# Kernel optimization log

Measured on AMD Instinct MI355X. Metric: run time of the kernel, lower is better.

## Reference

```python
import jax, jax.numpy as jnp
import numpy as np
from jax import lax

H_IMG, W_IMG = 1280, 1280
STRIDES = (8, 16, 32, 64, 128)
FEAT_SHAPES = tuple((H_IMG // s) * (W_IMG // s) for s in STRIDES)  # (25600,6400,1600,400,100)
N_POINTS = sum(FEAT_SHAPES)  # 34100
NUM_CLASSES = 1
TOPK = 1000
SCORE_THRESH = 0.05
NMS_THRESH = 0.5
MAX_DET = 300
BATCH = 8
N_GT = 200


def make_points():
    # matches AnchorFreePS.reference_points: cell centers at stride*i + stride//2, (cx, cy) order
    pts = []
    for s in STRIDES:
        h, w = H_IMG // s, W_IMG // s
        cx = np.arange(w, dtype=np.float32) * s + s // 2
        cy = np.arange(h, dtype=np.float32) * s + s // 2
        gy, gx = np.meshgrid(cy, cx, indexing='ij')
        pts.append(np.stack([gx, gy], axis=-1).reshape(-1, 2))
    return jnp.asarray(np.concatenate(pts, axis=0))


def setup_inputs() -> dict:
    key = jax.random.key(0)
    k1, k2, k3, k4 = jax.random.split(key, 4)
    points = make_points()  # [N,2]
    xy = jax.random.uniform(k1, (BATCH, N_GT, 2), minval=0.0, maxval=1000.0)
    wh = jax.random.uniform(k2, (BATCH, N_GT, 2), minval=20.0, maxval=260.0)
    gt_boxes = jnp.concatenate([xy, xy + wh], axis=-1)  # [B,M,4] x1y1x2y2
    cls_logits = jax.random.normal(k3, (BATCH, N_POINTS, NUM_CLASSES)) * 1.5 - 3.0
    regression = jax.random.uniform(k4, (BATCH, N_POINTS, 4)) * 0.1  # normalized ltrb codes
    return {"points": points, "gt_boxes": gt_boxes, "cls_logits": cls_logits, "regression": regression}


def match_points_to_boxes(points, gt_boxes):
    # point-in-box test + area-cost argmin (compute_loss matched_idxs)
    px = points[None, :, None, 0]  # [1,N,1]
    py = points[None, :, None, 1]
    b = gt_boxes[:, None, :, :]    # [B,1,M,4]
    inside = (px >= b[..., 0]) & (px <= b[..., 2]) & (py >= b[..., 1]) & (py <= b[..., 3])  # [B,N,M]
    matched = jnp.any(inside, axis=-1)  # [B,N]
    areas = (gt_boxes[..., 2] - gt_boxes[..., 0]) * (gt_boxes[..., 3] - gt_boxes[..., 1])  # [B,M]
    BIG = jnp.float32(2 ** 31 - 1)  # torch.iinfo(torch.int).max
    cost = jnp.where(inside, areas[:, None, :], BIG)
    idx = jnp.argmin(cost, axis=-1)
    return jnp.where(matched, idx, -1)


def decode_boxes(rel, pts):
    # FCOSBoxCoder.decode_single with weights (1,1,1,1)
    l = rel[:, 0] * W_IMG
    t = rel[:, 1] * H_IMG
    r = rel[:, 2] * W_IMG
    b = rel[:, 3] * H_IMG
    x, y = pts[:, 0], pts[:, 1]
    return jnp.stack([x - l, y - t, x + r, y + b], axis=-1)


def clip_boxes(boxes):
    return jnp.stack([
        jnp.clip(boxes[:, 0], 0.0, W_IMG),
        jnp.clip(boxes[:, 1], 0.0, H_IMG),
        jnp.clip(boxes[:, 2], 0.0, W_IMG),
        jnp.clip(boxes[:, 3], 0.0, H_IMG)], axis=-1)


def nms(boxes, scores, labels, valid_init):
    # fixed-size sequential NMS equivalent to batched_nms (same-label suppression)
    work = lax.stop_gradient(jnp.where(valid_init, scores, -jnp.inf))

    def body(w, _):
        i = jnp.argmax(w)
        s = w[i]
        box = boxes[i]
        x1 = jnp.maximum(box[0], boxes[:, 0])
        y1 = jnp.maximum(box[1], boxes[:, 1])
        x2 = jnp.minimum(box[2], boxes[:, 2])
        y2 = jnp.minimum(box[3], boxes[:, 3])
        inter = jnp.clip(x2 - x1, 0.0) * jnp.clip(y2 - y1, 0.0)
        a1 = (box[2] - box[0]) * (box[3] - box[1])
        a2 = (boxes[:, 2] - boxes[:, 0]) * (boxes[:, 3] - boxes[:, 1])
        iou = inter / (a1 + a2 - inter + 1e-9)
        supp = (iou > NMS_THRESH) & (labels == labels[i])
        w = jnp.where(supp, -jnp.inf, w).at[i].set(-jnp.inf)
        return w, (i, s)

    _, (idxs, picked) = lax.scan(body, work, None, length=MAX_DET)
    valid = picked > -jnp.inf
    return idxs, valid


def postprocess_image(points, cls_i, reg_i):
    bx_list, sc_list, lb_list = [], [], []
    off = 0
    for size in FEAT_SHAPES:  # fixed small level loop
        sl = slice(off, off + size)
        off += size
        scores = jax.nn.sigmoid(cls_i[sl]).reshape(-1)  # [size*C]
        k = min(TOPK, size * NUM_CLASSES)
        sc, idx = lax.top_k(scores, k)
        a = idx // NUM_CLASSES
        lb = idx % NUM_CLASSES
        bx = clip_boxes(decode_boxes(reg_i[sl][a], points[sl][a]))
        bx_list.append(bx)
        sc_list.append(sc)
        lb_list.append(lb)
    boxes = jnp.concatenate(bx_list, axis=0)
    scores = jnp.concatenate(sc_list, axis=0)
    labels = jnp.concatenate(lb_list, axis=0)
    idxs, valid = nms(boxes, scores, labels, scores > SCORE_THRESH)
    out_boxes = jnp.where(valid[:, None], boxes[idxs], 0.0)
    out_scores = jnp.where(valid, scores[idxs], 0.0)
    out_labels = jnp.where(valid, labels[idxs], -1)
    return out_boxes, out_scores, out_labels, valid


def reference(points, gt_boxes, cls_logits, regression):
    matched_idxs = match_points_to_boxes(points, gt_boxes)  # [B,N]
    boxes, scores, labels, valid = jax.vmap(
        lambda c, r: postprocess_image(points, c, r))(cls_logits, regression)
    return matched_idxs, boxes, scores, labels, valid
```

## Files before the change

kernel.cpp:

```cpp
#include <hip/hip_runtime.h>
#include <stdint.h>

#define N_POINTS   34100
#define BATCH      8
#define N_GT       200
#define NLEV       5
#define NCAND      3500
#define MAX_DET    300
#define SCORE_TH   0.05f
#define NMS_TH     0.5f
#define IMG        1280.0f
#define NBIN       4096
#define TIE_CAP    4096
#define MTH 0.50000002980232238769531250

#define OUT_MATCH  0
#define OUT_BOXES  272800
#define OUT_SCORES 282400
#define OUT_LABELS 284800
#define OUT_VALID  287200

#define WS_KEYS    0
#define WS_SBOX    2632192
#define WS_SSC     3080192
#define WS_MASK    3192192
#define WS_DIAG    9500032
#define WS_HIST    WS_MASK
#define HSUB       8
#define MASK_STRIDE 98560
#define DIAG_STRIDE 3520


typedef unsigned long long u64;
typedef uint32_t u32;

__device__ __forceinline__ int mask_off(int c) {
    int g = c >> 6;
    return 64 * (55 * g - (g * (g - 1)) / 2) + (c - (g << 6)) * (55 - g);
}

__device__ __forceinline__ int level_of(int p) {
    return (p < 25600) ? 0 : (p < 32000) ? 1 : (p < 33600) ? 2 : (p < 34000) ? 3 : 4;
}
__device__ __forceinline__ int loff_of(int l) {
    return (l == 0) ? 0 : (l == 1) ? 25600 : (l == 2) ? 32000 : (l == 3) ? 33600 : 34000;
}
__device__ __forceinline__ int k_of(int l) {
    return (l == 0) ? 1000 : (l == 1) ? 1000 : (l == 2) ? 1000 : (l == 3) ? 400 : 100;
}
__device__ __forceinline__ u64 readlane64(u64 v, int t) {
    u32 lo = (u32)__builtin_amdgcn_readlane((int)(u32)v, t);
    u32 hi = (u32)__builtin_amdgcn_readlane((int)(u32)(v >> 32), t);
    return ((u64)hi << 32) | lo;
}

#define MPT 2
__global__ __launch_bounds__(256)
void match_key_kernel(const float* __restrict__ points,
                      const float* __restrict__ gt,
                      float* __restrict__ out_match) {
#pragma clang fp contract(off)
    __shared__ float bx1[N_GT], by1[N_GT], bx2[N_GT], by2[N_GT], ar[N_GT];
    const int b = blockIdx.y;
    const int base = blockIdx.x * (256 * MPT) + threadIdx.x;

    for (int j = threadIdx.x; j < N_GT; j += 256) {
        float x1 = gt[(b * N_GT + j) * 4 + 0];
        float y1 = gt[(b * N_GT + j) * 4 + 1];
        float x2 = gt[(b * N_GT + j) * 4 + 2];
        float y2 = gt[(b * N_GT + j) * 4 + 3];
        bx1[j] = x1; by1[j] = y1; bx2[j] = x2; by2[j] = y2;
        ar[j] = (x2 - x1) * (y2 - y1);
    }
    __syncthreads();

    const float BIGF = 2147483648.0f;
    float px[MPT], py[MPT], best[MPT];
    int bi[MPT];
#pragma unroll
    for (int k = 0; k < MPT; ++k) {
        int p = base + k * 256;
        int pc = (p < N_POINTS) ? p : 0;
        px[k] = points[pc * 2 + 0];
        py[k] = points[pc * 2 + 1];
        best[k] = BIGF; bi[k] = -1;
    }
    for (int j = 0; j < N_GT; ++j) {
        float x1 = bx1[j], y1 = by1[j], x2 = bx2[j], y2 = by2[j], a = ar[j];
#pragma unroll
        for (int k = 0; k < MPT; ++k) {
            bool inside = (px[k] >= x1) && (px[k] <= x2) &&
                          (py[k] >= y1) && (py[k] <= y2);
            float cost = inside ? a : BIGF;
            if (cost < best[k]) { best[k] = cost; bi[k] = j; }
        }
    }
#pragma unroll
    for (int k = 0; k < MPT; ++k) {
        int p = base + k * 256;
        if (p >= N_POINTS) continue;
        out_match[b * N_POINTS + p] = (float)bi[k];
    }
}

__global__ __launch_bounds__(1024)
void hist_kernel(const float* __restrict__ logits,
                 u32* __restrict__ keys,
                 u32* __restrict__ ghist) {
#pragma clang fp contract(off)
    __shared__ u32 hh[NBIN];
    const int b = blockIdx.x & 7;
    const int f = blockIdx.x >> 3;
    const int tid = threadIdx.x;
    int lev, sub, p0, cnt;
    if (f < 8)       { lev = 0; sub = f;     p0 = f * 3200;             cnt = 3200; }
    else if (f < 10) { lev = 1; sub = f - 8; p0 = 25600 + (f - 8) * 3200; cnt = 3200; }
    else if (f == 10){ lev = 2; sub = 0;     p0 = 32000;                cnt = 1600; }
    else if (f == 11){ lev = 3; sub = 0;     p0 = 33600;                cnt = 400;  }
    else             { lev = 4; sub = 0;     p0 = 34000;                cnt = 100;  }

    for (int i = tid; i < NBIN; i += 1024) hh[i] = 0u;
    __syncthreads();

    for (int i = tid; i < cnt; i += 1024) {
        int p = p0 + i;
        float lg = logits[b * N_POINTS + p];
        float s = 1.0f / (1.0f + expf(-lg));
        u32 u = __float_as_uint(s);
        u32 key = (u & 0x80000000u) ? ~u : (u | 0x80000000u);
        keys[b * N_POINTS + p] = key;
        atomicAdd(&hh[(key >> 19) & 4095u], 1u);
    }
    __syncthreads();

    u32* outp = ghist + (((u32)b * NLEV + (u32)lev) * HSUB + (u32)sub) * NBIN;
    for (int i = tid; i < NBIN; i += 1024) outp[i] = hh[i];
}

#define SORT_T 1024
#define LSWZ(j) (((j) & 63) * 65 + ((j) >> 6))
__global__ __launch_bounds__(SORT_T)
void pipeline_kernel(const u32* __restrict__ keys,
                     const u32* __restrict__ ghist,
                     const float* __restrict__ reg,
                     const float* __restrict__ points,
                     float* __restrict__ sboxes,
                     float* __restrict__ sscores) {
#pragma clang fp contract(off)
    __shared__ __align__(16) char smem[131072];
    u64* sk   = (u64*)smem;
    u64* tb   = (u64*)(smem + 32768);
    u64* aux  = (u64*)(smem + 65536);
    u32* h    = (u32*)(smem + 98304);
    u32* bs   = (u32*)(smem + 114688);
    u32* lsb  = (u32*)smem;
    __shared__ u32 sTl[NLEV], skkl[NLEV], wt[16];
    __shared__ u32 scnt, stcnt;

    const int b = blockIdx.x;
    const int tid = threadIdx.x;
    const int lane = tid & 63;
    const int wid = tid >> 6;
    const u32* kk_ = keys + b * N_POINTS;

    if (tid == 0) { scnt = 0u; stcnt = 0u; }

    {
        const u32* hb = ghist + (u32)b * (NLEV * HSUB * NBIN);
#pragma unroll
        for (int lev = 0; lev < NLEV; ++lev) {
            const int SUBS = (lev == 0) ? 8 : (lev == 1) ? 2 : 1;
            const u32* hl = hb + lev * HSUB * NBIN + tid;
            u32 s0 = 0, s1 = 0, s2 = 0, s3 = 0;
#pragma unroll
            for (int sub = 0; sub < SUBS; ++sub) {
                const u32* hs = hl + sub * NBIN;
                s0 += hs[0]; s1 += hs[1024]; s2 += hs[2048]; s3 += hs[3072];
            }
            u32* lv = lsb + lev * 4160;
            lv[LSWZ(tid)]        = s0;
            lv[LSWZ(tid + 1024)] = s1;
            lv[LSWZ(tid + 2048)] = s2;
            lv[LSWZ(tid + 3072)] = s3;
        }
        const uint4* kp4 = (const uint4*)kk_;
        u32 wacc = 0;
        for (int i = tid; i < 8525; i += SORT_T) {
            uint4 v = kp4[i];
            wacc ^= v.x ^ v.y ^ v.z ^ v.w;
        }
        asm volatile("" :: "v"(wacc));
    }
    __syncthreads();

    if (wid < NLEV) {
        const u32 K = (u32)k_of(wid);
        const u32* hh = lsb + wid * 4160;
        u32 S = 0;
#pragma unroll 16
        for (int i = 0; i < 64; ++i) S += hh[i * 65 + lane];
        u32 acc = S;
#pragma unroll
        for (int off = 1; off < 64; off <<= 1) {
            u32 v = (u32)__shfl_down((int)acc, off);
            if (lane + off < 64) acc += v;
        }
        u32 sfxAfter = acc - S;
        bool hit = (sfxAfter < K) && (sfxAfter + S >= K);
        u64 bal = __ballot(hit);
        int Lg = (int)__builtin_ctzll(bal);
        u32 sfxG = (u32)__shfl((int)sfxAfter, Lg);

        u32 v = hh[lane * 65 + Lg];
        u32 acc2 = v;
#pragma unroll
        for (int off = 1; off < 64; off <<= 1) {
            u32 t = (u32)__shfl_down((int)acc2, off);
            if (lane + off < 64) acc2 += t;
        }
        u32 sfx2 = sfxG + acc2 - v;
        bool hit2 = (sfx2 < K) && (sfx2 + v >= K);
        if (hit2) { sTl[wid] = (u32)(Lg * 64 + lane); skkl[wid] = K - sfx2; }
    }
    __syncthreads();

    const u64 below = (lane == 0) ? 0ull : (~0ull >> (64 - lane));
    const int CHUNK = 4 * SORT_T;
    for (int it = 0; it < (N_POINTS + CHUNK - 1) / CHUNK; ++it) {
        u32 key4[4]; int pc4[4]; bool act4[4];
#pragma unroll
        for (int u = 0; u < 4; ++u) {
            int i = it * CHUNK + u * SORT_T + tid;
            act4[u] = (i < N_POINTS);
            pc4[u] = act4[u] ? i : (N_POINTS - 1);
            key4[u] = kk_[pc4[u]];
        }
#pragma unroll
        for (int u = 0; u < 4; ++u) {
            bool active = act4[u];
            int pc = pc4[u];
            u32 key = key4[u];
            int l = level_of(pc);
            u32 digit = (key >> 19) & 4095u;
            u32 T = sTl[l];
            bool isDef = active && (digit > T);
            bool isTie = active && (digit == T);
            u64 k50 = ((u64)key << 18) | ((u64)(7 - l) << 15)
                    | (u64)(32767 - (pc - loff_of(l)));
            u64 grp = __ballot(isDef);
            if (grp) {
                int leader = (int)__builtin_ctzll(grp);
                u32 base_ = 0;
                if (lane == leader)
                    base_ = atomicAdd(&scnt, (u32)__builtin_popcountll(grp));
                base_ = (u32)__shfl((int)base_, leader);
                if (isDef) sk[base_ + (u32)__builtin_popcountll(grp & below)] = k50;
            }
            u64 tg = __ballot(isTie);
            if (tg) {
                int leader = (int)__builtin_ctzll(tg);
                u32 base_ = 0;
                if (lane == leader)
                    base_ = atomicAdd(&stcnt, (u32)__builtin_popcountll(tg));
                base_ = (u32)__shfl((int)base_, leader);
                if (isTie) {
                    u32 pos = base_ + (u32)__builtin_popcountll(tg & below);
                    if (pos < TIE_CAP) tb[pos] = k50;
                }
            }
        }
    }
    __syncthreads();

    int t = (int)stcnt; if (t > TIE_CAP) t = TIE_CAP;
    for (int j0 = tid; j0 - tid < t; j0 += SORT_T) {
        bool active = j0 < t;
        u64 kj = active ? tb[j0] : 0ull;
        u32 lvtag = (u32)(kj >> 15) & 7u;
        int r = 0;
        for (int i = 0; i < t; ++i) {
            u64 ki = tb[i];
            r += (ki > kj && (((u32)(ki >> 15) & 7u) == lvtag)) ? 1 : 0;
        }
        bool inc = active && (r < (int)skkl[7 - lvtag]);
        u64 grp = __ballot(inc);
        if (grp) {
            int leader = (int)__builtin_ctzll(grp);
            u32 base_ = 0;
            if (lane == leader)
                base_ = atomicAdd(&scnt, (u32)__builtin_popcountll(grp));
            base_ = (u32)__shfl((int)base_, leader);
            if (inc) sk[base_ + (u32)__builtin_popcountll(grp & below)] = kj;
        }
    }
    __syncthreads();
    const int total = (int)scnt;

    for (int i = tid; i < NBIN; i += SORT_T) h[i] = 0u;
    __syncthreads();
    for (int i = tid; i < total; i += SORT_T)
        atomicAdd(&h[(u32)(sk[i] >> 37) & 4095u], 1u);
    __syncthreads();

    u32 t0 = h[4095 - 4 * tid];
    u32 t1 = h[4095 - (4 * tid + 1)];
    u32 t2 = h[4095 - (4 * tid + 2)];
    u32 t3 = h[4095 - (4 * tid + 3)];
    u32 tsum = t0 + t1 + t2 + t3;
    u32 sc_ = tsum;
#pragma unroll
    for (int off = 1; off < 64; off <<= 1) {
        u32 v = (u32)__shfl_up((int)sc_, off);
        if (lane >= off) sc_ += v;
    }
    if (lane == 63) wt[wid] = sc_;
    __syncthreads();
    if (tid < 64) {
        u32 v = (tid < 16) ? wt[tid] : 0u;
        u32 s2 = v;
#pragma unroll
        for (int off = 1; off < 16; off <<= 1) {
            u32 x = (u32)__shfl_up((int)s2, off);
            if (tid >= off) s2 += x;
        }
        if (tid < 16) wt[tid] = s2 - v;
    }
    __syncthreads();
    u32 run = (sc_ - tsum) + wt[wid];
    bs[4095 - 4 * tid] = run;       run += t0;
    bs[4095 - (4 * tid + 1)] = run; run += t1;
    bs[4095 - (4 * tid + 2)] = run; run += t2;
    bs[4095 - (4 * tid + 3)] = run;
    __syncthreads();
    for (int i = tid; i < NBIN; i += SORT_T) h[i] = 0u;
    __syncthreads();
    for (int i = tid; i < total; i += SORT_T) {
        u64 k = sk[i];
        u32 d = (u32)(k >> 37) & 4095u;
        u32 pos = bs[d] + atomicAdd(&h[d], 1u);
        aux[pos] = k;
    }
    __syncthreads();
    for (int p = tid; p < total; p += SORT_T) {
        u64 kp = aux[p];
        u32 d = (u32)(kp >> 37) & 4095u;
        u32 gbase = bs[d];
        u32 gend = (d == 0) ? (u32)total : bs[d - 1];
        u32 r = 0;
        for (u32 q = gbase; q < gend; ++q) r += (aux[q] > kp) ? 1u : 0u;
        sk[gbase + r] = kp;
    }
    __syncthreads();

    for (int r = tid; r < NCAND; r += SORT_T) {
        float x1 = 0.f, y1 = 0.f, x2 = 0.f, y2 = 0.f, sc = 0.f;
        if (r < total) {
            u64 k50 = sk[r];
            int lowb = (int)(k50 & 0x3FFFFull);
            int l = 7 - (lowb >> 15);
            int idxl = 32767 - (lowb & 32767);
            int p = loff_of(l) + idxl;
            u32 key32 = (u32)(k50 >> 18);
            sc = __uint_as_float(key32 ^ 0x80000000u);
            int gp = b * N_POINTS + p;
            float l_ = reg[gp * 4 + 0] * IMG;
            float t_ = reg[gp * 4 + 1] * IMG;
            float r_ = reg[gp * 4 + 2] * IMG;
            float bb = reg[gp * 4 + 3] * IMG;
            float px = points[p * 2 + 0];
            float py = points[p * 2 + 1];
            x1 = fminf(fmaxf(px - l_, 0.0f), IMG);
            y1 = fminf(fmaxf(py - t_, 0.0f), IMG);
            x2 = fminf(fmaxf(px + r_, 0.0f), IMG);
            y2 = fminf(fmaxf(py + bb, 0.0f), IMG);
        }
        int slot = b * NCAND + r;
        sboxes[slot * 4 + 0] = x1;
        sboxes[slot * 4 + 1] = y1;
        sboxes[slot * 4 + 2] = x2;
        sboxes[slot * 4 + 3] = y2;
        sscores[slot] = sc;
    }
}

__global__ __launch_bounds__(256)
void mask_kernel(const float* __restrict__ sboxes,
                 const float* __restrict__ sscores,
                 u64* __restrict__ mask,
                 u64* __restrict__ diag) {
#pragma clang fp contract(off)
    const int b = blockIdx.x & 7;
    const int gx = blockIdx.x >> 3;
    const int wv = threadIdx.x >> 6;
    const int lane = threadIdx.x & 63;
    const int NG = (NCAND + 3) >> 2;
    const int NH = (NG + 1) >> 1;
    const int gidx = gx * 4 + wv;
    if (gidx >= NH) return;

    const float4* gb = (const float4*)sboxes + b * NCAND;
    const float* gs = sscores + b * NCAND;
    u64* mout = mask + (size_t)b * MASK_STRIDE;
    u64* dout = diag + (size_t)b * DIAG_STRIDE;

    for (int s = 0; s < 2; ++s) {
        const int g0 = (s == 0) ? gidx : (NG - 1 - gidx);
        if (s == 1 && g0 == gidx) break;
        const int c0 = g0 << 2;

        float4 bc[4]; float a1[4]; bool ok[4]; int g[4]; u64* rp[4];
        bool any = false;
#pragma unroll
        for (int i = 0; i < 4; ++i) {
            int c = c0 + i;
            int cc = (c < NCAND) ? c : (NCAND - 1);
            bc[i] = gb[cc];
            a1[i] = (bc[i].z - bc[i].x) * (bc[i].w - bc[i].y);
            ok[i] = (c < NCAND) && (gs[cc] > SCORE_TH);
            g[i] = cc >> 6;
            rp[i] = mout + mask_off(cc) - g[i];
            any |= ok[i];
        }
        if (!any) continue;

        for (int w = (c0 >> 6); w < 55; ++w) {
            int cj = (w << 6) + lane;
            float4 bj = (cj < NCAND) ? gb[cj] : make_float4(0.f, 0.f, 0.f, 0.f);
            float a2 = (bj.z - bj.x) * (bj.w - bj.y);
#pragma unroll
            for (int i = 0; i < 4; ++i) {
                float x1 = fmaxf(bc[i].x, bj.x);
                float y1 = fmaxf(bc[i].y, bj.y);
                float x2 = fminf(bc[i].z, bj.z);
                float y2 = fminf(bc[i].w, bj.w);
                float inter = fmaxf(x2 - x1, 0.f) * fmaxf(y2 - y1, 0.f);
                float denom = a1[i] + a2 - inter + 1e-9f;
                float hf = 0.5f * denom;
                float rr = fmaf(0x1p-25f, denom, hf);
                u64 bits = __ballot(inter > rr);
                u64 eq = __ballot(inter == rr);
                if (eq) {
                    u64 fb = __ballot((double)inter > MTH * (double)denom);
                    bits |= (eq & fb);
                }
                if (lane == 0 && ok[i] && w >= g[i]) {
                    rp[i][w] = bits;
                    if (w == g[i]) dout[c0 + i] = bits;
                }
            }
        }
    }
}

__global__ __launch_bounds__(1024)
void scan_kernel(const float* __restrict__ sboxes,
                 const float* __restrict__ sscores,
                 const u64* __restrict__ mask,
                 const u64* __restrict__ diag,
                 float* __restrict__ out) {
    __shared__ u32 pick_idx[MAX_DET];
    const int b = blockIdx.x;
    const int tid = threadIdx.x;
    const u64* mrow = mask + (size_t)b * MASK_STRIDE;
    const u64* drow = diag + (size_t)b * DIAG_STRIDE;

    if (tid >= 64) {
        const uint4* mp = (const uint4*)mrow;
        const uint4* dp = (const uint4*)drow;
        const int t = tid - 64;
        u32 a0 = 0, a1 = 0, a2 = 0, a3 = 0;
        int i = t;
        for (; i + 2880 < 49280; i += 3840) {
            uint4 v0 = mp[i];
            uint4 v1 = mp[i + 960];
            uint4 v2 = mp[i + 1920];
            uint4 v3 = mp[i + 2880];
            a0 ^= v0.x ^ v0.y ^ v0.z ^ v0.w;
            a1 ^= v1.x ^ v1.y ^ v1.z ^ v1.w;
            a2 ^= v2.x ^ v2.y ^ v2.z ^ v2.w;
            a3 ^= v3.x ^ v3.y ^ v3.z ^ v3.w;
        }
        for (; i < 49280; i += 960) {
            uint4 v = mp[i];
            a0 ^= v.x ^ v.y ^ v.z ^ v.w;
        }
        if (t < 880) {
            uint4 v0 = dp[t];
            uint4 v1 = dp[t + 880];
            a1 ^= v0.x ^ v0.y ^ v0.z ^ v0.w;
            a2 ^= v1.x ^ v1.y ^ v1.z ^ v1.w;
        }
        u32 acc = a0 ^ a1 ^ a2 ^ a3;
        asm volatile("" :: "v"(acc));
        return;
    }

    const int lane = tid;
    const float4* gb = (const float4*)sboxes + b * NCAND;
    const float* gs = sscores + b * NCAND;

    float* ob = out + OUT_BOXES  + b * MAX_DET * 4;
    float* os = out + OUT_SCORES + b * MAX_DET;
    float* ol = out + OUT_LABELS + b * MAX_DET;
    float* ov = out + OUT_VALID  + b * MAX_DET;

    u64 m = 0ull;
    u64 rowN = drow[lane];
    float sjN = gs[lane];

    int kept = 0;
    for (int w = 0; w < 55; ++w) {
        const int wbase = w << 6;
        const u64 row = rowN;
        const float sj = sjN;
        if (w < 54) {
            int cn = wbase + 64 + lane;
            int cc = (cn < NCAND) ? cn : (NCAND - 1);
            rowN = drow[cc];
            float s = gs[cc];
            sjN = (cn < NCAND) ? s : 0.f;
        }
        int c = wbase + lane;
        u64 bad = __ballot(!((c < NCAND) && (sj > SCORE_TH)));
        u64 cur = readlane64(m, w) | bad;
        u64 km = 0ull;
        while (kept < MAX_DET) {
            u64 avail = ~cur;
            if (avail == 0ull) break;
            int t = (int)__builtin_ctzll(avail);
            u64 r = readlane64(row, t);
            cur |= r | (1ull << t);
            km |= 1ull << t;
            if (lane == 0) pick_idx[kept] = (u32)(wbase + t);
            kept++;
        }
        if (km) {
            const bool lr = (lane >= w && lane < 55);
            const int lo = lane - w;
            u64 acc = 0ull;
            while (km) {
#define POPBIT(tn) int tn = -1; if (km) { tn = (int)__builtin_ctzll(km); km &= km - 1ull; }
                POPBIT(t0) POPBIT(t1) POPBIT(t2) POPBIT(t3)
                POPBIT(t4) POPBIT(t5) POPBIT(t6) POPBIT(t7)
#undef POPBIT
                u64 v0 = 0, v1 = 0, v2 = 0, v3 = 0, v4 = 0, v5 = 0, v6 = 0, v7 = 0;
                if (lr) {
                    v0 = mrow[mask_off(wbase + t0) + lo];
                    if (t1 >= 0) v1 = mrow[mask_off(wbase + t1) + lo];
                    if (t2 >= 0) v2 = mrow[mask_off(wbase + t2) + lo];
                    if (t3 >= 0) v3 = mrow[mask_off(wbase + t3) + lo];
                    if (t4 >= 0) v4 = mrow[mask_off(wbase + t4) + lo];
                    if (t5 >= 0) v5 = mrow[mask_off(wbase + t5) + lo];
                    if (t6 >= 0) v6 = mrow[mask_off(wbase + t6) + lo];
                    if (t7 >= 0) v7 = mrow[mask_off(wbase + t7) + lo];
                }
                acc |= ((v0 | v1) | (v2 | v3)) | ((v4 | v5) | (v6 | v7));
            }
            m |= acc;
        }
        if (kept >= MAX_DET) break;
    }

    for (int k = lane; k < kept; k += 64) {
        u32 c = pick_idx[k];
        float4 bx = gb[c];
        float s = gs[c];
        ob[k * 4 + 0] = bx.x;
        ob[k * 4 + 1] = bx.y;
        ob[k * 4 + 2] = bx.z;
        ob[k * 4 + 3] = bx.w;
        os[k] = s;
        ol[k] = 0.0f;
        ov[k] = 1.0f;
    }
    for (int k = kept + lane; k < MAX_DET; k += 64) {
        ob[k * 4 + 0] = 0.f; ob[k * 4 + 1] = 0.f;
        ob[k * 4 + 2] = 0.f; ob[k * 4 + 3] = 0.f;
        os[k] = 0.f; ol[k] = -1.f; ov[k] = 0.f;
    }
}

extern "C" void kernel_launch(void* const* d_in, const int* in_sizes, int n_in,
                              void* d_out, int out_size, void* d_ws, size_t ws_size,
                              hipStream_t stream) {
    const float* points = (const float*)d_in[0];
    const float* gt     = (const float*)d_in[1];
    const float* logits = (const float*)d_in[2];
    const float* reg    = (const float*)d_in[3];
    float* out = (float*)d_out;

    u32* keys      = (u32*)((char*)d_ws + WS_KEYS);
    float* sboxes  = (float*)((char*)d_ws + WS_SBOX);
    float* sscores = (float*)((char*)d_ws + WS_SSC);
    u64* mask   = (u64*)((char*)d_ws + WS_MASK);
    u64* diag   = (u64*)((char*)d_ws + WS_DIAG);
    u32* ghist  = (u32*)((char*)d_ws + WS_HIST);

    dim3 g1((N_POINTS + 256 * MPT - 1) / (256 * MPT), BATCH);
    match_key_kernel<<<g1, 256, 0, stream>>>(points, gt, out + OUT_MATCH);

    hist_kernel<<<13 * BATCH, 1024, 0, stream>>>(logits, keys, ghist);

    pipeline_kernel<<<BATCH, SORT_T, 0, stream>>>(keys, ghist, reg, points,
                                                  sboxes, sscores);

    mask_kernel<<<110 * BATCH, 256, 0, stream>>>(sboxes, sscores, mask, diag);

    scan_kernel<<<BATCH, 1024, 0, stream>>>(sboxes, sscores, mask, diag, out);
}
```

Before: 227.9 us.

## Merge match and histogram kernels, split threshold select from compaction kernel

Combines the point-to-box matching kernel and the score histogram kernel into one launch whose blocks branch by index, so the independent matching work and histogram work can run concurrently on the GPU. The histogram threshold selection moves out of the big pipeline kernel into its own small kernel that writes thresholds into spare workspace, and the compaction kernel reads them back. Cache-warming prefetch loops are widened to more loads in flight and extended to the box and score buffers. This adds an extra kernel launch and a global round-trip for the thresholds, and relies on an unused histogram slot as scratch space.

After: 230.0 us. No clear change (+0.9%).

```diff
diff --git a/kernel.cpp b/kernel.cpp
--- a/kernel.cpp
+++ b/kernel.cpp
@@ -54,116 +54,98 @@
     return ((u64)hi << 32) | lo;
 }
 
-#define MPT 2
-__global__ __launch_bounds__(256)
-void match_key_kernel(const float* __restrict__ points,
-                      const float* __restrict__ gt,
-                      float* __restrict__ out_match) {
+__global__ __launch_bounds__(1024)
+void match_hist_kernel(const float* __restrict__ points,
+                       const float* __restrict__ gt,
+                       const float* __restrict__ logits,
+                       float* __restrict__ out_match,
+                       u32* __restrict__ keys,
+                       u32* __restrict__ ghist) {
 #pragma clang fp contract(off)
     __shared__ float bx1[N_GT], by1[N_GT], bx2[N_GT], by2[N_GT], ar[N_GT];
-    const int b = blockIdx.y;
-    const int base = blockIdx.x * (256 * MPT) + threadIdx.x;
-
-    for (int j = threadIdx.x; j < N_GT; j += 256) {
-        float x1 = gt[(b * N_GT + j) * 4 + 0];
-        float y1 = gt[(b * N_GT + j) * 4 + 1];
-        float x2 = gt[(b * N_GT + j) * 4 + 2];
-        float y2 = gt[(b * N_GT + j) * 4 + 3];
-        bx1[j] = x1; by1[j] = y1; bx2[j] = x2; by2[j] = y2;
-        ar[j] = (x2 - x1) * (y2 - y1);
-    }
-    __syncthreads();
-
-    const float BIGF = 2147483648.0f;
-    float px[MPT], py[MPT], best[MPT];
-    int bi[MPT];
-#pragma unroll
-    for (int k = 0; k < MPT; ++k) {
-        int p = base + k * 256;
-        int pc = (p < N_POINTS) ? p : 0;
-        px[k] = points[pc * 2 + 0];
-        py[k] = points[pc * 2 + 1];
-        best[k] = BIGF; bi[k] = -1;
-    }
-    for (int j = 0; j < N_GT; ++j) {
-        float x1 = bx1[j], y1 = by1[j], x2 = bx2[j], y2 = by2[j], a = ar[j];
-#pragma unroll
-        for (int k = 0; k < MPT; ++k) {
-            bool inside = (px[k] >= x1) && (px[k] <= x2) &&
-                          (py[k] >= y1) && (py[k] <= y2);
-            float cost = inside ? a : BIGF;
-            if (cost < best[k]) { best[k] = cost; bi[k] = j; }
-        }
-    }
-#pragma unroll
-    for (int k = 0; k < MPT; ++k) {
-        int p = base + k * 256;
-        if (p >= N_POINTS) continue;
-        out_match[b * N_POINTS + p] = (float)bi[k];
-    }
-}
-
-__global__ __launch_bounds__(1024)
-void hist_kernel(const float* __restrict__ logits,
-                 u32* __restrict__ keys,
-                 u32* __restrict__ ghist) {
-#pragma clang fp contract(off)
     __shared__ u32 hh[NBIN];
     const int b = blockIdx.x & 7;
-    const int f = blockIdx.x >> 3;
+    const int g = blockIdx.x >> 3;
     const int tid = threadIdx.x;
-    int lev, sub, p0, cnt;
-    if (f < 8)       { lev = 0; sub = f;     p0 = f * 3200;             cnt = 3200; }
-    else if (f < 10) { lev = 1; sub = f - 8; p0 = 25600 + (f - 8) * 3200; cnt = 3200; }
-    else if (f == 10){ lev = 2; sub = 0;     p0 = 32000;                cnt = 1600; }
-    else if (f == 11){ lev = 3; sub = 0;     p0 = 33600;                cnt = 400;  }
-    else             { lev = 4; sub = 0;     p0 = 34000;                cnt = 100;  }
-
-    for (int i = tid; i < NBIN; i += 1024) hh[i] = 0u;
-    __syncthreads();
-
-    for (int i = tid; i < cnt; i += 1024) {
-        int p = p0 + i;
-        float lg = logits[b * N_POINTS + p];
-        float s = 1.0f / (1.0f + expf(-lg));
-        u32 u = __float_as_uint(s);
-        u32 key = (u & 0x80000000u) ? ~u : (u | 0x80000000u);
-        keys[b * N_POINTS + p] = key;
-        atomicAdd(&hh[(key >> 19) & 4095u], 1u);
-    }
-    __syncthreads();
-
-    u32* outp = ghist + (((u32)b * NLEV + (u32)lev) * HSUB + (u32)sub) * NBIN;
-    for (int i = tid; i < NBIN; i += 1024) outp[i] = hh[i];
-}
-
-#define SORT_T 1024
+
+    if (g < 17) {
+        const int base = g * 2048 + tid;
+        for (int j = tid; j < N_GT; j += 1024) {
+            float x1 = gt[(b * N_GT + j) * 4 + 0];
+            float y1 = gt[(b * N_GT + j) * 4 + 1];
+            float x2 = gt[(b * N_GT + j) * 4 + 2];
+            float y2 = gt[(b * N_GT + j) * 4 + 3];
+            bx1[j] = x1; by1[j] = y1; bx2[j] = x2; by2[j] = y2;
+            ar[j] = (x2 - x1) * (y2 - y1);
+        }
+        __syncthreads();
+
+        const float BIGF = 2147483648.0f;
+        float px[2], py[2], best[2];
+        int bi[2];
+#pragma unroll
+        for (int k = 0; k < 2; ++k) {
+            int p = base + k * 1024;
+            int pc = (p < N_POINTS) ? p : 0;
+            px[k] = points[pc * 2 + 0];
+            py[k] = points[pc * 2 + 1];
+            best[k] = BIGF; bi[k] = -1;
+        }
+        for (int j = 0; j < N_GT; ++j) {
+            float x1 = bx1[j], y1 = by1[j], x2 = bx2[j], y2 = by2[j], a = ar[j];
+#pragma unroll
+            for (int k = 0; k < 2; ++k) {
+                bool inside = (px[k] >= x1) && (px[k] <= x2) &&
+                              (py[k] >= y1) && (py[k] <= y2);
+                float cost = inside ? a : BIGF;
+                if (cost < best[k]) { best[k] = cost; bi[k] = j; }
+            }
+        }
+#pragma unroll
+        for (int k = 0; k < 2; ++k) {
+            int p = base + k * 1024;
+            if (p >= N_POINTS) continue;
+            out_match[b * N_POINTS + p] = (float)bi[k];
+        }
+    } else {
+        const int f = g - 17;
+        int lev, sub, p0, cnt;
+        if (f < 8)       { lev = 0; sub = f;     p0 = f * 3200;               cnt = 3200; }
+        else if (f < 10) { lev = 1; sub = f - 8; p0 = 25600 + (f - 8) * 3200; cnt = 3200; }
+        else if (f == 10){ lev = 2; sub = 0;     p0 = 32000;                  cnt = 1600; }
+        else if (f == 11){ lev = 3; sub = 0;     p0 = 33600;                  cnt = 400;  }
+        else             { lev = 4; sub = 0;     p0 = 34000;                  cnt = 100;  }
+
+        for (int i = tid; i < NBIN; i += 1024) hh[i] = 0u;
+        __syncthreads();
+
+        for (int i = tid; i < cnt; i += 1024) {
+            int p = p0 + i;
+            float lg = logits[b * N_POINTS + p];
+            float s = 1.0f / (1.0f + expf(-lg));
+            u32 u = __float_as_uint(s);
+            u32 key = (u & 0x80000000u) ? ~u : (u | 0x80000000u);
+            keys[b * N_POINTS + p] = key;
+            atomicAdd(&hh[(key >> 19) & 4095u], 1u);
+        }
+        __syncthreads();
+
+        u32* outp = ghist + (((u32)b * NLEV + (u32)lev) * HSUB + (u32)sub) * NBIN;
+        for (int i = tid; i < NBIN; i += 1024) outp[i] = hh[i];
+    }
+}
+
+#define SEL_OFF(b) ((((u32)(b) * NLEV + 4) * HSUB + 7) * NBIN)
+
 #define LSWZ(j) (((j) & 63) * 65 + ((j) >> 6))
-__global__ __launch_bounds__(SORT_T)
-void pipeline_kernel(const u32* __restrict__ keys,
-                     const u32* __restrict__ ghist,
-                     const float* __restrict__ reg,
-                     const float* __restrict__ points,
-                     float* __restrict__ sboxes,
-                     float* __restrict__ sscores) {
-#pragma clang fp contract(off)
-    __shared__ __align__(16) char smem[131072];
-    u64* sk   = (u64*)smem;
-    u64* tb   = (u64*)(smem + 32768);
-    u64* aux  = (u64*)(smem + 65536);
-    u32* h    = (u32*)(smem + 98304);
-    u32* bs   = (u32*)(smem + 114688);
-    u32* lsb  = (u32*)smem;
-    __shared__ u32 sTl[NLEV], skkl[NLEV], wt[16];
-    __shared__ u32 scnt, stcnt;
-
+__global__ __launch_bounds__(1024)
+void select_kernel(u32* __restrict__ ghist) {
+    __shared__ u32 lsb[5 * 4160];
+    __shared__ u32 sTl[NLEV], skkl[NLEV];
     const int b = blockIdx.x;
     const int tid = threadIdx.x;
     const int lane = tid & 63;
     const int wid = tid >> 6;
-    const u32* kk_ = keys + b * N_POINTS;
-
-    if (tid == 0) { scnt = 0u; stcnt = 0u; }
 
     {
         const u32* hb = ghist + (u32)b * (NLEV * HSUB * NBIN);
@@ -183,13 +165,6 @@
             lv[LSWZ(tid + 2048)] = s2;
             lv[LSWZ(tid + 3072)] = s3;
         }
-        const uint4* kp4 = (const uint4*)kk_;
-        u32 wacc = 0;
-        for (int i = tid; i < 8525; i += SORT_T) {
-            uint4 v = kp4[i];
-            wacc ^= v.x ^ v.y ^ v.z ^ v.w;
-        }
-        asm volatile("" :: "v"(wacc));
     }
     __syncthreads();
 
@@ -221,6 +196,66 @@
         u32 sfx2 = sfxG + acc2 - v;
         bool hit2 = (sfx2 < K) && (sfx2 + v >= K);
         if (hit2) { sTl[wid] = (u32)(Lg * 64 + lane); skkl[wid] = K - sfx2; }
+    }
+    __syncthreads();
+    if (tid < NLEV) {
+        u32* selp = ghist + SEL_OFF(b);
+        selp[tid] = sTl[tid];
+        selp[NLEV + tid] = skkl[tid];
+    }
+}
+
+#define SORT_T 1024
+__global__ __launch_bounds__(SORT_T)
+void compact_kernel(const u32* __restrict__ keys,
+                    const u32* __restrict__ ghist,
+                    const float* __restrict__ reg,
+                    const float* __restrict__ points,
+                    float* __restrict__ sboxes,
+                    float* __restrict__ sscores) {
+#pragma clang fp contract(off)
+    __shared__ __align__(16) char smem[131072];
+    u64* sk   = (u64*)smem;
+    u64* tb   = (u64*)(smem + 32768);
+    u64* aux  = (u64*)(smem + 65536);
+    u32* h    = (u32*)(smem + 98304);
+    u32* bs   = (u32*)(smem + 114688);
+    __shared__ u32 sTl[NLEV], skkl[NLEV], wt[16];
+    __shared__ u32 scnt, stcnt;
+
+    const int b = blockIdx.x;
+    const int tid = threadIdx.x;
+    const int lane = tid & 63;
+    const int wid = tid >> 6;
+    const u32* kk_ = keys + b * N_POINTS;
+
+    if (tid == 0) { scnt = 0u; stcnt = 0u; }
+    if (tid < NLEV) {
+        const u32* selp = ghist + SEL_OFF(b);
+        sTl[tid] = selp[tid];
+        skkl[tid] = selp[NLEV + tid];
+    }
+
+    {
+        const uint4* kp4 = (const uint4*)kk_;
+        u32 a0 = 0, a1 = 0, a2 = 0, a3 = 0;
+        int i = tid;
+        for (; i + 3072 < 8525; i += 4096) {
+            uint4 v0 = kp4[i];
+            uint4 v1 = kp4[i + 1024];
+            uint4 v2 = kp4[i + 2048];
+            uint4 v3 = kp4[i + 3072];
+            a0 ^= v0.x ^ v0.y ^ v0.z ^ v0.w;
+            a1 ^= v1.x ^ v1.y ^ v1.z ^ v1.w;
+            a2 ^= v2.x ^ v2.y ^ v2.z ^ v2.w;
+            a3 ^= v3.x ^ v3.y ^ v3.z ^ v3.w;
+        }
+        for (; i < 8525; i += 1024) {
+            uint4 v = kp4[i];
+            a0 ^= v.x ^ v.y ^ v.z ^ v.w;
+        }
+        u32 wacc = a0 ^ a1 ^ a2 ^ a3;
+        asm volatile("" :: "v"(wacc));
     }
     __syncthreads();
 
@@ -463,22 +498,34 @@
     const int tid = threadIdx.x;
     const u64* mrow = mask + (size_t)b * MASK_STRIDE;
     const u64* drow = diag + (size_t)b * DIAG_STRIDE;
+    const float4* gb = (const float4*)sboxes + b * NCAND;
+    const float* gs = sscores + b * NCAND;
 
     if (tid >= 64) {
         const uint4* mp = (const uint4*)mrow;
         const uint4* dp = (const uint4*)drow;
+        const uint4* bp = (const uint4*)gb;
+        const uint4* sp = (const uint4*)gs;
         const int t = tid - 64;
-        u32 a0 = 0, a1 = 0, a2 = 0, a3 = 0;
+        u32 a0 = 0, a1 = 0, a2 = 0, a3 = 0, a4 = 0, a5 = 0, a6 = 0, a7 = 0;
         int i = t;
-        for (; i + 2880 < 49280; i += 3840) {
+        for (; i + 6720 < 49280; i += 7680) {
             uint4 v0 = mp[i];
             uint4 v1 = mp[i + 960];
             uint4 v2 = mp[i + 1920];
             uint4 v3 = mp[i + 2880];
+            uint4 v4 = mp[i + 3840];
+            uint4 v5 = mp[i + 4800];
+            uint4 v6 = mp[i + 5760];
+            uint4 v7 = mp[i + 6720];
             a0 ^= v0.x ^ v0.y ^ v0.z ^ v0.w;
             a1 ^= v1.x ^ v1.y ^ v1.z ^ v1.w;
             a2 ^= v2.x ^ v2.y ^ v2.z ^ v2.w;
             a3 ^= v3.x ^ v3.y ^ v3.z ^ v3.w;
+            a4 ^= v4.x ^ v4.y ^ v4.z ^ v4.w;
+            a5 ^= v5.x ^ v5.y ^ v5.z ^ v5.w;
+            a6 ^= v6.x ^ v6.y ^ v6.z ^ v6.w;
+            a7 ^= v7.x ^ v7.y ^ v7.z ^ v7.w;
         }
         for (; i < 49280; i += 960) {
             uint4 v = mp[i];
@@ -490,14 +537,20 @@
             a1 ^= v0.x ^ v0.y ^ v0.z ^ v0.w;
             a2 ^= v1.x ^ v1.y ^ v1.z ^ v1.w;
         }
-        u32 acc = a0 ^ a1 ^ a2 ^ a3;
+        for (int j = t; j < 3500; j += 960) {
+            uint4 v = bp[j];
+            a3 ^= v.x ^ v.y ^ v.z ^ v.w;
+        }
+        if (t < 875) {
+            uint4 v = sp[t];
+            a4 ^= v.x ^ v.y ^ v.z ^ v.w;
+        }
+        u32 acc = (a0 ^ a1) ^ (a2 ^ a3) ^ (a4 ^ a5) ^ (a6 ^ a7);
         asm volatile("" :: "v"(acc));
         return;
     }
 
     const int lane = tid;
-    const float4* gb = (const float4*)sboxes + b * NCAND;
-    const float* gs = sscores + b * NCAND;
 
     float* ob = out + OUT_BOXES  + b * MAX_DET * 4;
     float* os = out + OUT_SCORES + b * MAX_DET;
@@ -596,13 +649,13 @@
     u64* diag   = (u64*)((char*)d_ws + WS_DIAG);
     u32* ghist  = (u32*)((char*)d_ws + WS_HIST);
 
-    dim3 g1((N_POINTS + 256 * MPT - 1) / (256 * MPT), BATCH);
-    match_key_kernel<<<g1, 256, 0, stream>>>(points, gt, out + OUT_MATCH);
-
-    hist_kernel<<<13 * BATCH, 1024, 0, stream>>>(logits, keys, ghist);
-
-    pipeline_kernel<<<BATCH, SORT_T, 0, stream>>>(keys, ghist, reg, points,
-                                                  sboxes, sscores);
+    match_hist_kernel<<<30 * BATCH, 1024, 0, stream>>>(points, gt, logits,
+                                                       out + OUT_MATCH, keys, ghist);
+
+    select_kernel<<<BATCH, 1024, 0, stream>>>(ghist);
+
+    compact_kernel<<<BATCH, SORT_T, 0, stream>>>(keys, ghist, reg, points,
+                                                 sboxes, sscores);
 
     mask_kernel<<<110 * BATCH, 256, 0, stream>>>(sboxes, sscores, mask, diag);
 
```
